# Optimization experiments

Hardware: AMD Instinct MI355X
Metric: run time of the kernel (lower is better)

The kernel has to match this reference:

```python
import jax, jax.numpy as jnp
import numpy as np

T, B, D, FF, Z = 1024, 32, 512, 2048, 64


def _trunc_normal(key, shape, std=0.001):
    return std * jax.random.truncated_normal(key, -2.0, 2.0, shape, dtype=jnp.float32)


def setup_inputs() -> dict:
    key = jax.random.key(0)
    ks = jax.random.split(key, 16)
    inp = {
        "x": jax.random.normal(ks[0], (T, B, D), dtype=jnp.float32),
        "first": jax.random.bernoulli(ks[1], 0.05, (T, B)),  # episode boundaries
        "h0": jax.random.normal(ks[2], (B, D), dtype=jnp.float32),
        "c0": jax.random.normal(ks[3], (B, D), dtype=jnp.float32),
        # pre-LN params
        "ln_g": jnp.ones((D,), jnp.float32),
        "ln_b": jnp.zeros((D,), jnp.float32),
        # LSTM params (PyTorch gate order i,f,g,o)
        "Wih": jax.random.normal(ks[4], (4 * D, D), jnp.float32) / np.sqrt(D),
        "Whh": jax.random.normal(ks[5], (4 * D, D), jnp.float32) / np.sqrt(D),
        "bih": jnp.zeros((4 * D,), jnp.float32),
        "bhh": jnp.zeros((4 * D,), jnp.float32),
        # pointwise FFN: mlp0 = Linear(D,FF)+ReLU, mlp1 = Linear(FF,D)
        "mlp0_w": jax.random.normal(ks[6], (FF, D), jnp.float32) / np.sqrt(D),
        "mlp0_b": jnp.zeros((FF,), jnp.float32),
        "mlp1_w": jax.random.normal(ks[7], (D, FF), jnp.float32) / np.sqrt(FF),
        "mlp1_b": jnp.zeros((D,), jnp.float32),
        # adapter bottleneck (trunc-normal init, std=0.001)
        "aw0": _trunc_normal(ks[8], (Z, D)),
        "ab0": _trunc_normal(ks[9], (Z,)),
        "aw1": _trunc_normal(ks[10], (D, Z)),
        "ab1": _trunc_normal(ks[11], (D,)),
    }
    return inp


def _layernorm(x, g, b, eps=1e-5):
    mu = jnp.mean(x, axis=-1, keepdims=True)
    var = jnp.mean(jnp.square(x - mu), axis=-1, keepdims=True)
    return (x - mu) * jax.lax.rsqrt(var + eps) * g + b


def _lstm_scan(x, first, h0, c0, Wih, Whh, bih, bhh):
    # x: [T,B,D], first: [T,B] bool resets state before the step
    def step(carry, inp):
        h, c = carry
        xt, ft = inp
        keep = jnp.where(ft, 0.0, 1.0)[:, None].astype(h.dtype)
        h = h * keep
        c = c * keep
        gates = xt @ Wih.T + bih + h @ Whh.T + bhh  # [B,4D]
        i, f, g, o = jnp.split(gates, 4, axis=-1)
        c = jax.nn.sigmoid(f) * c + jax.nn.sigmoid(i) * jnp.tanh(g)
        h = jax.nn.sigmoid(o) * jnp.tanh(c)
        return (h, c), h
    (h, c), ys = jax.lax.scan(step, (h0, c0), (x, first))
    return ys, h, c


def reference(x, first, h0, c0, ln_g, ln_b, Wih, Whh, bih, bhh,
              mlp0_w, mlp0_b, mlp1_w, mlp1_b, aw0, ab0, aw1, ab1):
    residual = x
    xn = _layernorm(x, ln_g, ln_b)
    y, h_out, c_out = _lstm_scan(xn, first, h0, c0, Wih, Whh, bih, bhh)
    y = y + residual  # is_residual and 'lstm' in recurrence_type
    residual = y
    # pointwise layer: mlp1(mlp0(y)) with mlp0 = Linear+ReLU
    y = jax.nn.relu(y @ mlp0_w.T + mlp0_b) @ mlp1_w.T + mlp1_b
    # adapter: y + net(y)
    y = y + jax.nn.relu(y @ aw0.T + ab0) @ aw1.T + ab1
    y = y + residual
    return (y, h_out, c_out)
```

## Files before the change

kernel.cpp:

```cpp
#include <hip/hip_runtime.h>

#define T_ 1024
#define B_ 32
#define D_ 512
#define FF_ 2048
#define TB_ 32768
#define TCH_ 256
#define RCH_ 8192

typedef short bf16x8 __attribute__((ext_vector_type(8)));
typedef float f32x4 __attribute__((ext_vector_type(4)));

static __device__ __forceinline__ unsigned int pack2bf(float a, float b){
  union { __bf16 h[2]; unsigned int u; } z;
  z.h[0] = (__bf16)a; z.h[1] = (__bf16)b; return z.u;
}
static __device__ __forceinline__ float bflo(unsigned int u){ return __uint_as_float(u<<16); }
static __device__ __forceinline__ float bfhi(unsigned int u){ return __uint_as_float(u & 0xffff0000u); }
static __device__ __forceinline__ float sigm(float x){ return 1.f/(1.f+__expf(-x)); }
static __device__ __forceinline__ float tanh_(float x){ return 1.f - 2.f/(1.f+__expf(2.f*x)); }

static __device__ __forceinline__ bool firstval(const void* p, int mode, int idx){
  return mode ? (((const int*)p)[idx] != 0) : (((const unsigned char*)p)[idx] != 0);
}

__global__ void detect_first_kernel(const unsigned char* __restrict__ p, unsigned int* __restrict__ mode){
  __shared__ int found;
  if (threadIdx.x == 0) found = 0;
  __syncthreads();
  int f = 0;
  for (int i = threadIdx.x; i < TB_; i += 256) if ((i & 3) != 0 && p[i] != 0) f = 1;
  if (f) atomicAdd(&found, 1);
  __syncthreads();
  if (threadIdx.x == 0) *mode = (found == 0) ? 1u : 0u;
}

__global__ void convert_w_kernel(const float* __restrict__ Wih, const float* __restrict__ Whh,
                                 const float* __restrict__ m0w, const float* __restrict__ m1w,
                                 const float* __restrict__ aw0, const float* __restrict__ aw1,
                                 __bf16* __restrict__ Wihb, __bf16* __restrict__ Whhb,
                                 __bf16* __restrict__ m0b,  __bf16* __restrict__ m1b,
                                 __bf16* __restrict__ awT0, __bf16* __restrict__ awT1){
  int bid = blockIdx.x;
  if (bid < 4096) {
    int ai = bid >> 10;
    size_t off = (size_t)(bid & 1023) * 1024 + threadIdx.x * 4;
    const float* src = (ai==0)?Wih:(ai==1)?Whh:(ai==2)?m0w:m1w;
    __bf16* dst = (ai==0)?Wihb:(ai==1)?Whhb:(ai==2)?m0b:m1b;
    float4 v = *(const float4*)(src + off);
    union { __bf16 h[4]; uint2 u; } z;
    z.h[0]=(__bf16)v.x; z.h[1]=(__bf16)v.y; z.h[2]=(__bf16)v.z; z.h[3]=(__bf16)v.w;
    *(uint2*)(void*)(dst + off) = z.u;
  } else {
    int e = (bid - 4096) * 256 + threadIdx.x;
    if (e < 32768) { int k = e >> 6, j = e & 63;  awT0[e] = (__bf16)aw0[j*512 + k]; }
    else { int e2 = e - 32768; int j = e2 >> 9, d = e2 & 511; awT1[e2] = (__bf16)aw1[d*64 + j]; }
  }
}

__global__ __launch_bounds__(256) void ln_kernel(const float* __restrict__ x,
                                                 const float* __restrict__ g, const float* __restrict__ b,
                                                 __bf16* __restrict__ xn){
  const int w = threadIdx.x >> 6, l = threadIdx.x & 63;
  const int row = blockIdx.x * 4 + w;
  const float* xr = x + (size_t)row * D_;
  const int e0 = l * 4, e1 = 256 + l * 4;
  float4 v0 = *(const float4*)(xr + e0);
  float4 v1 = *(const float4*)(xr + e1);
  float s  = v0.x+v0.y+v0.z+v0.w + v1.x+v1.y+v1.z+v1.w;
  float s2 = v0.x*v0.x+v0.y*v0.y+v0.z*v0.z+v0.w*v0.w + v1.x*v1.x+v1.y*v1.y+v1.z*v1.z+v1.w*v1.w;
  #pragma unroll
  for (int off = 1; off < 64; off <<= 1) { s += __shfl_xor(s, off); s2 += __shfl_xor(s2, off); }
  float mu = s * (1.f/512.f);
  float var = s2 * (1.f/512.f) - mu*mu;
  float rstd = rsqrtf(var + 1e-5f);
  float4 g0 = *(const float4*)(g + e0), g1 = *(const float4*)(g + e1);
  float4 b0 = *(const float4*)(b + e0), b1 = *(const float4*)(b + e1);
  union { __bf16 h[4]; uint2 u; } o0, o1;
  o0.h[0]=(__bf16)((v0.x-mu)*rstd*g0.x+b0.x); o0.h[1]=(__bf16)((v0.y-mu)*rstd*g0.y+b0.y);
  o0.h[2]=(__bf16)((v0.z-mu)*rstd*g0.z+b0.z); o0.h[3]=(__bf16)((v0.w-mu)*rstd*g0.w+b0.w);
  o1.h[0]=(__bf16)((v1.x-mu)*rstd*g1.x+b1.x); o1.h[1]=(__bf16)((v1.y-mu)*rstd*g1.y+b1.y);
  o1.h[2]=(__bf16)((v1.z-mu)*rstd*g1.z+b1.z); o1.h[3]=(__bf16)((v1.w-mu)*rstd*g1.w+b1.w);
  *(uint2*)(void*)(xn + (size_t)row * D_ + e0) = o0.u;
  *(uint2*)(void*)(xn + (size_t)row * D_ + e1) = o1.u;
}

template<int RELU, int BF16OUT, int TWOBIAS>
__global__ __launch_bounds__(256) void gemm_bt(const __bf16* __restrict__ A, const __bf16* __restrict__ W,
                                               const float* __restrict__ bias0, const float* __restrict__ bias1,
                                               float* __restrict__ Cf, __bf16* __restrict__ Cb,
                                               int M, int N, int K){
  __shared__ __bf16 As[128*64];
  __shared__ __bf16 Bs[128*64];
  const int tid = threadIdx.x, w = tid >> 6, l = tid & 63;
  const int bm = blockIdx.x, bn = blockIdx.y;
  const int wm = (w >> 1) * 64, wn = (w & 1) * 64;
  const int nk = K >> 6;

  uint4 ra[4], rb[4];
  #pragma unroll
  for (int i = 0; i < 4; ++i) {
    int s = tid + (i << 8); int row = s >> 3; int ks = s & 7;
    ra[i] = *(const uint4*)(void*)(A + (size_t)(bm*128 + row) * K + ks*8);
    rb[i] = *(const uint4*)(void*)(W + (size_t)(bn*128 + row) * K + ks*8);
  }
  f32x4 acc[4][4];
  #pragma unroll
  for (int mt = 0; mt < 4; ++mt)
    #pragma unroll
    for (int nt = 0; nt < 4; ++nt) acc[mt][nt] = (f32x4){0.f,0.f,0.f,0.f};

  for (int kt = 0; kt < nk; ++kt) {
    __syncthreads();
    #pragma unroll
    for (int i = 0; i < 4; ++i) {
      int s = tid + (i << 8); int row = s >> 3; int ks = s & 7;
      int wi = row * 64 + ((ks * 8) ^ ((row & 7) << 3));
      *(uint4*)(void*)(As + wi) = ra[i];
      *(uint4*)(void*)(Bs + wi) = rb[i];
    }
    __syncthreads();
    if (kt + 1 < nk) {
      #pragma unroll
      for (int i = 0; i < 4; ++i) {
        int s = tid + (i << 8); int row = s >> 3; int ks = s & 7;
        ra[i] = *(const uint4*)(void*)(A + (size_t)(bm*128 + row) * K + (kt+1)*64 + ks*8);
        rb[i] = *(const uint4*)(void*)(W + (size_t)(bn*128 + row) * K + (kt+1)*64 + ks*8);
      }
    }
    #pragma unroll
    for (int kk = 0; kk < 2; ++kk) {
      bf16x8 af[4], bfv[4];
      const int ke = kk * 32 + ((l >> 4) << 3);
      #pragma unroll
      for (int mt = 0; mt < 4; ++mt) {
        int row = wm + mt*16 + (l & 15);
        af[mt] = *(const bf16x8*)(void*)(As + row*64 + (ke ^ ((row & 7) << 3)));
      }
      #pragma unroll
      for (int nt = 0; nt < 4; ++nt) {
        int row = wn + nt*16 + (l & 15);
        bfv[nt] = *(const bf16x8*)(void*)(Bs + row*64 + (ke ^ ((row & 7) << 3)));
      }
      #pragma unroll
      for (int mt = 0; mt < 4; ++mt)
        #pragma unroll
        for (int nt = 0; nt < 4; ++nt)
          acc[mt][nt] = __builtin_amdgcn_mfma_f32_16x16x32_bf16(af[mt], bfv[nt], acc[mt][nt], 0, 0, 0);
    }
  }
  #pragma unroll
  for (int nt = 0; nt < 4; ++nt) {
    int c = bn*128 + wn + nt*16 + (l & 15);
    float bv = bias0[c];
    if (TWOBIAS) bv += bias1[c];
    #pragma unroll
    for (int mt = 0; mt < 4; ++mt) {
      #pragma unroll
      for (int j = 0; j < 4; ++j) {
        int r = bm*128 + wm + mt*16 + ((l >> 4) << 2) + j;
        float v = acc[mt][nt][j] + bv;
        if (RELU) v = fmaxf(v, 0.f);
        if (BF16OUT) Cb[(size_t)r * N + c] = (__bf16)v;
        else         Cf[(size_t)r * N + c] = v;
      }
    }
  }
}

__global__ __launch_bounds__(512) void lstm_scan(
    const __bf16* __restrict__ Whh,
    const __bf16* __restrict__ preC,
    const float*  __restrict__ x,
    const void*   __restrict__ firstp,
    const float*  __restrict__ h0,
    const float*  __restrict__ c0,
    float*        __restrict__ cstate,
    __bf16*       __restrict__ ymidbC,
    unsigned long long* __restrict__ HP,
    const unsigned int* __restrict__ modep,
    float* __restrict__ hout, float* __restrict__ cout,
    int tBase){
  const int s = blockIdx.x, tid = threadIdx.x, w = tid >> 6, l = tid & 63;
  const int d0 = s * 32;
  __shared__ __bf16 Hl[32 * 512];
  __shared__ float  gl[32 * 132];
  const int mode = (int)*modep;

  bf16x8 wf[16];
  {
    int rl = w*16 + (l & 15);
    int gr = (rl >> 5) * 512 + d0 + (rl & 31);
    const __bf16* base = Whh + (size_t)gr * 512 + ((l >> 4) << 3);
    #pragma unroll
    for (int kt = 0; kt < 16; ++kt) wf[kt] = *(const bf16x8*)(void*)(base + kt*32);
  }
  const int b = tid >> 4, dl2 = (tid & 15) * 2;
  const int dg = d0 + dl2;
  const int opid = b * 256 + s * 16 + (tid & 15);

  float cr[2];
  if (tBase == 0) {
    float k0 = firstval(firstp, mode, b) ? 0.f : 1.f;
    float2 c2 = *(const float2*)(c0 + (size_t)b*512 + dg);
    cr[0] = c2.x * k0; cr[1] = c2.y * k0;
    float2 h = *(const float2*)(h0 + (size_t)b*512 + dg);
    unsigned long long pkt = (1ULL << 32) | (unsigned long long)pack2bf(h.x*k0, h.y*k0);
    __hip_atomic_store(HP + opid, pkt, __ATOMIC_RELAXED, __HIP_MEMORY_SCOPE_AGENT);
  } else {
    float2 c2 = *(const float2*)(cstate + (size_t)b*512 + dg);
    cr[0] = c2.x; cr[1] = c2.y;
  }

  for (int tl = 0; tl < TCH_; ++tl) {
    const int t = tBase + tl;
    const int rowg = t * 32 + b, rowl = tl * 32 + b;
    unsigned int pg[4];
    #pragma unroll
    for (int gi = 0; gi < 4; ++gi)
      pg[gi] = *(const unsigned int*)(void*)(preC + (size_t)rowl * 2048 + gi*512 + dg);
    float2 xv = *(const float2*)(x + (size_t)rowg * 512 + dg);
    const bool f_t1 = (t < T_-1) ? firstval(firstp, mode, rowg + 32) : false;

    const unsigned want = (unsigned)(t + 1);
    const unsigned long long* Pb = HP + ((size_t)(t & 1) << 13);
    unsigned long long pk[16];
    #pragma unroll
    for (int j = 0; j < 16; ++j)
      pk[j] = __hip_atomic_load(Pb + tid + (j << 9), __ATOMIC_RELAXED, __HIP_MEMORY_SCOPE_AGENT);
    while (true) {
      unsigned stale = 0;
      #pragma unroll
      for (int j = 0; j < 16; ++j)
        if ((unsigned)(pk[j] >> 32) != want) stale |= (1u << j);
      if (!stale) break;
      __builtin_amdgcn_s_sleep(1);
      #pragma unroll
      for (int j = 0; j < 16; ++j)
        if (stale & (1u << j))
          pk[j] = __hip_atomic_load(Pb + tid + (j << 9), __ATOMIC_RELAXED, __HIP_MEMORY_SCOPE_AGENT);
    }
    #pragma unroll
    for (int j = 0; j < 16; ++j) {
      int pid = tid + (j << 9);
      int pb = pid >> 8, ps = (pid >> 4) & 15, pi = pid & 15;
      int q = ps*32 + pi*2;
      *(unsigned int*)(void*)(Hl + pb*512 + (q ^ ((pb & 7) << 3))) = (unsigned)pk[j];
    }
    __syncthreads();

    f32x4 a0a = (f32x4){0.f,0.f,0.f,0.f}, a0b = (f32x4){0.f,0.f,0.f,0.f};
    f32x4 a1a = (f32x4){0.f,0.f,0.f,0.f}, a1b = (f32x4){0.f,0.f,0.f,0.f};
    #pragma unroll
    for (int kt = 0; kt < 16; kt += 2) {
      int ke0 = kt*32 + ((l >> 4) << 3), ke1 = (kt+1)*32 + ((l >> 4) << 3);
      int r0 = (l & 15), r1 = 16 + (l & 15);
      bf16x8 h00 = *(const bf16x8*)(void*)(Hl + r0*512 + (ke0 ^ ((r0 & 7) << 3)));
      bf16x8 h01 = *(const bf16x8*)(void*)(Hl + r0*512 + (ke1 ^ ((r0 & 7) << 3)));
      bf16x8 h10 = *(const bf16x8*)(void*)(Hl + r1*512 + (ke0 ^ ((r1 & 7) << 3)));
      bf16x8 h11 = *(const bf16x8*)(void*)(Hl + r1*512 + (ke1 ^ ((r1 & 7) << 3)));
      a0a = __builtin_amdgcn_mfma_f32_16x16x32_bf16(h00, wf[kt],   a0a, 0, 0, 0);
      a0b = __builtin_amdgcn_mfma_f32_16x16x32_bf16(h01, wf[kt+1], a0b, 0, 0, 0);
      a1a = __builtin_amdgcn_mfma_f32_16x16x32_bf16(h10, wf[kt],   a1a, 0, 0, 0);
      a1b = __builtin_amdgcn_mfma_f32_16x16x32_bf16(h11, wf[kt+1], a1b, 0, 0, 0);
    }
    f32x4 acc0 = a0a + a0b, acc1 = a1a + a1b;
    {
      int col = w*16 + (l & 15);
      #pragma unroll
      for (int j = 0; j < 4; ++j) {
        gl[(((l >> 4) << 2) + j) * 132 + col]        = acc0[j];
        gl[((16 + ((l >> 4) << 2) + j)) * 132 + col] = acc1[j];
      }
    }
    __syncthreads();

    float2 gv[4];
    #pragma unroll
    for (int gi = 0; gi < 4; ++gi) gv[gi] = *(const float2*)(gl + b*132 + gi*32 + dl2);
    const float keep1 = f_t1 ? 0.f : 1.f;
    float hh[2], cc[2];
    #pragma unroll
    for (int p = 0; p < 2; ++p) {
      float gi_ = (p ? gv[0].y : gv[0].x) + (p ? bfhi(pg[0]) : bflo(pg[0]));
      float gf_ = (p ? gv[1].y : gv[1].x) + (p ? bfhi(pg[1]) : bflo(pg[1]));
      float gg_ = (p ? gv[2].y : gv[2].x) + (p ? bfhi(pg[2]) : bflo(pg[2]));
      float go_ = (p ? gv[3].y : gv[3].x) + (p ? bfhi(pg[3]) : bflo(pg[3]));
      float cn = sigm(gf_) * cr[p] + sigm(gi_) * tanh_(gg_);
      float h  = sigm(go_) * tanh_(cn);
      cc[p] = cn; hh[p] = h;
    }
    cr[0] = cc[0] * keep1; cr[1] = cc[1] * keep1;
    float2 yv = { hh[0] + xv.x, hh[1] + xv.y };
    if (t < T_-1) {
      unsigned long long pkt = (((unsigned long long)(unsigned)(t + 2)) << 32)
                             | (unsigned long long)pack2bf(hh[0]*keep1, hh[1]*keep1);
      __hip_atomic_store(HP + (((size_t)((t+1) & 1)) << 13) + opid, pkt,
                         __ATOMIC_RELAXED, __HIP_MEMORY_SCOPE_AGENT);
      if (tl == TCH_-1) *(float2*)(cstate + (size_t)b*512 + dg) = make_float2(cr[0], cr[1]);
    } else {
      *(float2*)(hout + (size_t)b*512 + dg) = make_float2(hh[0], hh[1]);
      *(float2*)(cout + (size_t)b*512 + dg) = make_float2(cc[0], cc[1]);
    }
    *(unsigned int*)(void*)(ymidbC + (size_t)rowl * 512 + dg) = pack2bf(yv.x, yv.y);
  }
}

__global__ __launch_bounds__(256) void adapter_out_kernel(
    float* __restrict__ y2,
    const __bf16* __restrict__ ymidb,
    const __bf16* __restrict__ awT0,
    const __bf16* __restrict__ awT1,
    const float* __restrict__ ab0, const float* __restrict__ ab1){
  __shared__ float zl[16 * 64];
  const int w = threadIdx.x >> 6, l = threadIdx.x & 63;
  const int r0 = blockIdx.x * 16;
  const float bz = ab0[l];
  #pragma unroll
  for (int rr = 0; rr < 4; ++rr) {
    int rowl = w*4 + rr;
    const float* yr = y2 + (size_t)(r0 + rowl) * 512;
    float acc = bz;
    #pragma unroll 4
    for (int k = 0; k < 512; ++k) acc += yr[k] * (float)awT0[k*64 + l];
    zl[rowl*64 + l] = fmaxf(acc, 0.f);
  }
  __syncthreads();
  #pragma unroll
  for (int rr = 0; rr < 4; ++rr) {
    int rowl = w*4 + rr; int row = r0 + rowl;
    const float* yr = y2  + (size_t)row * 512;
    const __bf16* mr = ymidb + (size_t)row * 512;
    #pragma unroll
    for (int dd = 0; dd < 8; ++dd) {
      int d = dd*64 + l;
      float acc = ab1[d] + yr[d] + (float)mr[d];
      #pragma unroll 4
      for (int j = 0; j < 64; ++j) acc += zl[rowl*64 + j] * (float)awT1[j*512 + d];
      y2[(size_t)row * 512 + d] = acc;
    }
  }
}

extern "C" void kernel_launch(void* const* d_in, const int* in_sizes, int n_in,
                              void* d_out, int out_size, void* d_ws, size_t ws_size,
                              hipStream_t stream){
  (void)in_sizes; (void)n_in; (void)out_size; (void)ws_size;
  const float* x    = (const float*)d_in[0];
  const void*  first=               d_in[1];
  const float* h0   = (const float*)d_in[2];
  const float* c0   = (const float*)d_in[3];
  const float* ln_g = (const float*)d_in[4];
  const float* ln_b = (const float*)d_in[5];
  const float* Wih  = (const float*)d_in[6];
  const float* Whh  = (const float*)d_in[7];
  const float* bih  = (const float*)d_in[8];
  const float* bhh  = (const float*)d_in[9];
  const float* m0w  = (const float*)d_in[10];
  const float* m0b  = (const float*)d_in[11];
  const float* m1w  = (const float*)d_in[12];
  const float* m1b  = (const float*)d_in[13];
  const float* aw0  = (const float*)d_in[14];
  const float* ab0  = (const float*)d_in[15];
  const float* aw1  = (const float*)d_in[16];
  const float* ab1  = (const float*)d_in[17];

  char* ws = (char*)d_ws;
  __bf16* buf0  = (__bf16*)(ws + 0LL);
  __bf16* xnbfC = (__bf16*)(ws + 33554432LL);
  __bf16* ymidbC= (__bf16*)(ws + 41943040LL);
  __bf16* wihb  = (__bf16*)(ws + 50331648LL);
  __bf16* whhb  = (__bf16*)(ws + 52428800LL);
  __bf16* m0bf  = (__bf16*)(ws + 54525952LL);
  __bf16* m1bf  = (__bf16*)(ws + 56623104LL);
  __bf16* awT0  = (__bf16*)(ws + 58720256LL);
  __bf16* awT1  = (__bf16*)(ws + 58785792LL);
  unsigned long long* HP = (unsigned long long*)(ws + 58851328LL);
  float*  cstate= (float*) (ws + 58982400LL);
  unsigned int* mode = (unsigned int*)(ws + 59047936LL);
  __bf16* preC = buf0;
  __bf16* a1C  = buf0;

  float* out  = (float*)d_out;
  float* hout = out + (size_t)TB_ * D_;
  float* cout = hout + B_ * D_;

  hipMemsetAsync(HP, 0, 131072, stream);
  detect_first_kernel<<<1, 256, 0, stream>>>((const unsigned char*)first, mode);
  convert_w_kernel<<<4352, 256, 0, stream>>>(Wih, Whh, m0w, m1w, aw0, aw1,
                                             wihb, whhb, m0bf, m1bf, awT0, awT1);
  for (int c = 0; c < 4; ++c) {
    const size_t ro = (size_t)c * RCH_;
    ln_kernel<<<RCH_/4, 256, 0, stream>>>(x + ro * D_, ln_g, ln_b, xnbfC);
    gemm_bt<0,1,1><<<dim3(RCH_/128, FF_/128), 256, 0, stream>>>(xnbfC, wihb, bih, bhh,
                                                                nullptr, preC, RCH_, 2048, 512);
    lstm_scan<<<16, 512, 0, stream>>>(whhb, preC, x, first, h0, c0, cstate, ymidbC,
                                      HP, mode, hout, cout, c * TCH_);
    gemm_bt<1,1,0><<<dim3(RCH_/128, FF_/128), 256, 0, stream>>>(ymidbC, m0bf, m0b, nullptr,
                                                                nullptr, a1C, RCH_, FF_, 512);
    gemm_bt<0,0,0><<<dim3(RCH_/128, D_/128), 256, 0, stream>>>(a1C, m1bf, m1b, nullptr,
                                                               out + ro * D_, nullptr, RCH_, D_, FF_);
    adapter_out_kernel<<<RCH_/16, 256, 0, stream>>>(out + ro * D_, ymidbC, awT0, awT1, ab0, ab1);
  }
}
```

Baseline: 5.378 ms.

## Overlap LSTM scan with previous chunk FFN and next chunk input GEMM

Fuses the per-chunk pipeline into one persistent-style launch. Blocks 0-15 run the recurrent scan for chunk c, blocks 16-79 run the FFN and adapter for chunk c-1, and blocks 80-143 compute layernorm plus the input projection for chunk c+1, with double-buffered workspace. LayerNorm is folded into the input GEMM's A-tile load, and the FFN panel chains both GEMMs and the adapter per 128-row panel. The aim is to hide the latency-bound scan behind the throughput-bound GEMMs, at the cost of 64-block GEMMs with low parallelism that may compete with the scan blocks, and a workspace-size fallback path.

```diff
diff --git a/kernel.cpp b/kernel.cpp
--- a/kernel.cpp
+++ b/kernel.cpp
@@ -10,6 +10,12 @@
 
 typedef short bf16x8 __attribute__((ext_vector_type(8)));
 typedef float f32x4 __attribute__((ext_vector_type(4)));
+
+union SharedU {
+  struct { __bf16 Hl[32*512]; float gl[32*132]; } s;
+  struct { __bf16 As[128*64]; __bf16 Bs[128*64]; float stat[256]; } g;
+  float zl[128*64];
+};
 
 static __device__ __forceinline__ unsigned int pack2bf(float a, float b){
   union { __bf16 h[2]; unsigned int u; } z;
@@ -58,79 +64,85 @@
   }
 }
 
-__global__ __launch_bounds__(256) void ln_kernel(const float* __restrict__ x,
-                                                 const float* __restrict__ g, const float* __restrict__ b,
-                                                 __bf16* __restrict__ xn){
-  const int w = threadIdx.x >> 6, l = threadIdx.x & 63;
-  const int row = blockIdx.x * 4 + w;
-  const float* xr = x + (size_t)row * D_;
-  const int e0 = l * 4, e1 = 256 + l * 4;
-  float4 v0 = *(const float4*)(xr + e0);
-  float4 v1 = *(const float4*)(xr + e1);
-  float s  = v0.x+v0.y+v0.z+v0.w + v1.x+v1.y+v1.z+v1.w;
-  float s2 = v0.x*v0.x+v0.y*v0.y+v0.z*v0.z+v0.w*v0.w + v1.x*v1.x+v1.y*v1.y+v1.z*v1.z+v1.w*v1.w;
+template<int RELU,int BF16OUT,int TWOBIAS,int AMODE>
+static __device__ void tile_gemm(SharedU& sh,
+    const __bf16* A, const float* Ax, const float* lng, const float* lnb,
+    const __bf16* W, const float* bias0, const float* bias1,
+    float* Cf, __bf16* Cb, int aRow0, int cRow0, int bn, int N, int K){
+  __bf16* As = sh.g.As; __bf16* Bs = sh.g.Bs; const float* stat = sh.g.stat;
+  const int tid = threadIdx.x, w = tid >> 6, l = tid & 63;
+  const int wm = (w >> 2) * 64, wn = (w & 3) * 32;
+  const int nk = K >> 6;
+  uint4 ra[2], rb[2];
+  float4 rx[2][2];
   #pragma unroll
-  for (int off = 1; off < 64; off <<= 1) { s += __shfl_xor(s, off); s2 += __shfl_xor(s2, off); }
-  float mu = s * (1.f/512.f);
-  float var = s2 * (1.f/512.f) - mu*mu;
-  float rstd = rsqrtf(var + 1e-5f);
-  float4 g0 = *(const float4*)(g + e0), g1 = *(const float4*)(g + e1);
-  float4 b0 = *(const float4*)(b + e0), b1 = *(const float4*)(b + e1);
-  union { __bf16 h[4]; uint2 u; } o0, o1;
-  o0.h[0]=(__bf16)((v0.x-mu)*rstd*g0.x+b0.x); o0.h[1]=(__bf16)((v0.y-mu)*rstd*g0.y+b0.y);
-  o0.h[2]=(__bf16)((v0.z-mu)*rstd*g0.z+b0.z); o0.h[3]=(__bf16)((v0.w-mu)*rstd*g0.w+b0.w);
-  o1.h[0]=(__bf16)((v1.x-mu)*rstd*g1.x+b1.x); o1.h[1]=(__bf16)((v1.y-mu)*rstd*g1.y+b1.y);
-  o1.h[2]=(__bf16)((v1.z-mu)*rstd*g1.z+b1.z); o1.h[3]=(__bf16)((v1.w-mu)*rstd*g1.w+b1.w);
-  *(uint2*)(void*)(xn + (size_t)row * D_ + e0) = o0.u;
-  *(uint2*)(void*)(xn + (size_t)row * D_ + e1) = o1.u;
-}
-
-template<int RELU, int BF16OUT, int TWOBIAS>
-__global__ __launch_bounds__(256) void gemm_bt(const __bf16* __restrict__ A, const __bf16* __restrict__ W,
-                                               const float* __restrict__ bias0, const float* __restrict__ bias1,
-                                               float* __restrict__ Cf, __bf16* __restrict__ Cb,
-                                               int M, int N, int K){
-  __shared__ __bf16 As[128*64];
-  __shared__ __bf16 Bs[128*64];
-  const int tid = threadIdx.x, w = tid >> 6, l = tid & 63;
-  const int bm = blockIdx.x, bn = blockIdx.y;
-  const int wm = (w >> 1) * 64, wn = (w & 1) * 64;
-  const int nk = K >> 6;
-
-  uint4 ra[4], rb[4];
-  #pragma unroll
-  for (int i = 0; i < 4; ++i) {
-    int s = tid + (i << 8); int row = s >> 3; int ks = s & 7;
-    ra[i] = *(const uint4*)(void*)(A + (size_t)(bm*128 + row) * K + ks*8);
+  for (int i = 0; i < 2; ++i) {
+    int s = tid + (i << 9); int row = s >> 3; int ks = s & 7;
+    if (AMODE == 2) {
+      const float* px = Ax + (size_t)(aRow0 + row) * 512 + ks*8;
+      rx[i][0] = *(const float4*)px; rx[i][1] = *(const float4*)(px + 4);
+    } else if (AMODE == 1) {
+      const unsigned long long* pa = (const unsigned long long*)(void*)(A + (size_t)(aRow0 + row) * K + ks*8);
+      union { unsigned long long q[2]; uint4 u; } z;
+      z.q[0] = __hip_atomic_load(pa,   __ATOMIC_RELAXED, __HIP_MEMORY_SCOPE_AGENT);
+      z.q[1] = __hip_atomic_load(pa+1, __ATOMIC_RELAXED, __HIP_MEMORY_SCOPE_AGENT);
+      ra[i] = z.u;
+    } else {
+      ra[i] = *(const uint4*)(void*)(A + (size_t)(aRow0 + row) * K + ks*8);
+    }
     rb[i] = *(const uint4*)(void*)(W + (size_t)(bn*128 + row) * K + ks*8);
   }
-  f32x4 acc[4][4];
+  f32x4 acc[4][2];
   #pragma unroll
   for (int mt = 0; mt < 4; ++mt)
     #pragma unroll
-    for (int nt = 0; nt < 4; ++nt) acc[mt][nt] = (f32x4){0.f,0.f,0.f,0.f};
+    for (int nt = 0; nt < 2; ++nt) acc[mt][nt] = (f32x4){0.f,0.f,0.f,0.f};
 
   for (int kt = 0; kt < nk; ++kt) {
     __syncthreads();
     #pragma unroll
-    for (int i = 0; i < 4; ++i) {
-      int s = tid + (i << 8); int row = s >> 3; int ks = s & 7;
+    for (int i = 0; i < 2; ++i) {
+      int s = tid + (i << 9); int row = s >> 3; int ks = s & 7;
       int wi = row * 64 + ((ks * 8) ^ ((row & 7) << 3));
-      *(uint4*)(void*)(As + wi) = ra[i];
+      if (AMODE == 2) {
+        float mu = stat[row], rs = stat[128 + row];
+        int col = kt*64 + ks*8;
+        float4 g0 = *(const float4*)(lng + col), g1 = *(const float4*)(lng + col + 4);
+        float4 b0 = *(const float4*)(lnb + col), b1 = *(const float4*)(lnb + col + 4);
+        union { __bf16 h[8]; uint4 u; } z;
+        z.h[0]=(__bf16)((rx[i][0].x-mu)*rs*g0.x+b0.x); z.h[1]=(__bf16)((rx[i][0].y-mu)*rs*g0.y+b0.y);
+        z.h[2]=(__bf16)((rx[i][0].z-mu)*rs*g0.z+b0.z); z.h[3]=(__bf16)((rx[i][0].w-mu)*rs*g0.w+b0.w);
+        z.h[4]=(__bf16)((rx[i][1].x-mu)*rs*g1.x+b1.x); z.h[5]=(__bf16)((rx[i][1].y-mu)*rs*g1.y+b1.y);
+        z.h[6]=(__bf16)((rx[i][1].z-mu)*rs*g1.z+b1.z); z.h[7]=(__bf16)((rx[i][1].w-mu)*rs*g1.w+b1.w);
+        *(uint4*)(void*)(As + wi) = z.u;
+      } else {
+        *(uint4*)(void*)(As + wi) = ra[i];
+      }
       *(uint4*)(void*)(Bs + wi) = rb[i];
     }
     __syncthreads();
     if (kt + 1 < nk) {
       #pragma unroll
-      for (int i = 0; i < 4; ++i) {
-        int s = tid + (i << 8); int row = s >> 3; int ks = s & 7;
-        ra[i] = *(const uint4*)(void*)(A + (size_t)(bm*128 + row) * K + (kt+1)*64 + ks*8);
+      for (int i = 0; i < 2; ++i) {
+        int s = tid + (i << 9); int row = s >> 3; int ks = s & 7;
+        if (AMODE == 2) {
+          const float* px = Ax + (size_t)(aRow0 + row) * 512 + (kt+1)*64 + ks*8;
+          rx[i][0] = *(const float4*)px; rx[i][1] = *(const float4*)(px + 4);
+        } else if (AMODE == 1) {
+          const unsigned long long* pa = (const unsigned long long*)(void*)(A + (size_t)(aRow0 + row) * K + (kt+1)*64 + ks*8);
+          union { unsigned long long q[2]; uint4 u; } z;
+          z.q[0] = __hip_atomic_load(pa,   __ATOMIC_RELAXED, __HIP_MEMORY_SCOPE_AGENT);
+          z.q[1] = __hip_atomic_load(pa+1, __ATOMIC_RELAXED, __HIP_MEMORY_SCOPE_AGENT);
+          ra[i] = z.u;
+        } else {
+          ra[i] = *(const uint4*)(void*)(A + (size_t)(aRow0 + row) * K + (kt+1)*64 + ks*8);
+        }
         rb[i] = *(const uint4*)(void*)(W + (size_t)(bn*128 + row) * K + (kt+1)*64 + ks*8);
       }
     }
     #pragma unroll
     for (int kk = 0; kk < 2; ++kk) {
-      bf16x8 af[4], bfv[4];
+      bf16x8 af[4], bfv[2];
       const int ke = kk * 32 + ((l >> 4) << 3);
       #pragma unroll
       for (int mt = 0; mt < 4; ++mt) {
@@ -138,19 +150,19 @@
         af[mt] = *(const bf16x8*)(void*)(As + row*64 + (ke ^ ((row & 7) << 3)));
       }
       #pragma unroll
-      for (int nt = 0; nt < 4; ++nt) {
+      for (int nt = 0; nt < 2; ++nt) {
         int row = wn + nt*16 + (l & 15);
         bfv[nt] = *(const bf16x8*)(void*)(Bs + row*64 + (ke ^ ((row & 7) << 3)));
       }
       #pragma unroll
       for (int mt = 0; mt < 4; ++mt)
         #pragma unroll
-        for (int nt = 0; nt < 4; ++nt)
+        for (int nt = 0; nt < 2; ++nt)
           acc[mt][nt] = __builtin_amdgcn_mfma_f32_16x16x32_bf16(af[mt], bfv[nt], acc[mt][nt], 0, 0, 0);
     }
   }
   #pragma unroll
-  for (int nt = 0; nt < 4; ++nt) {
+  for (int nt = 0; nt < 2; ++nt) {
     int c = bn*128 + wn + nt*16 + (l & 15);
     float bv = bias0[c];
     if (TWOBIAS) bv += bias1[c];
@@ -158,7 +170,7 @@
     for (int mt = 0; mt < 4; ++mt) {
       #pragma unroll
       for (int j = 0; j < 4; ++j) {
-        int r = bm*128 + wm + mt*16 + ((l >> 4) << 2) + j;
+        int r = cRow0 + wm + mt*16 + ((l >> 4) << 2) + j;
         float v = acc[mt][nt][j] + bv;
         if (RELU) v = fmaxf(v, 0.f);
         if (BF16OUT) Cb[(size_t)r * N + c] = (__bf16)v;
@@ -168,24 +180,84 @@
   }
 }
 
-__global__ __launch_bounds__(512) void lstm_scan(
-    const __bf16* __restrict__ Whh,
-    const __bf16* __restrict__ preC,
-    const float*  __restrict__ x,
-    const void*   __restrict__ firstp,
-    const float*  __restrict__ h0,
-    const float*  __restrict__ c0,
-    float*        __restrict__ cstate,
-    __bf16*       __restrict__ ymidbC,
-    unsigned long long* __restrict__ HP,
-    const unsigned int* __restrict__ modep,
-    float* __restrict__ hout, float* __restrict__ cout,
-    int tBase){
-  const int s = blockIdx.x, tid = threadIdx.x, w = tid >> 6, l = tid & 63;
+static __device__ void pre_panel(SharedU& sh, int panel, const float* x,
+                                 const float* lng, const float* lnb,
+                                 const __bf16* wihb, const float* bih, const float* bhh,
+                                 __bf16* preOut, int chunkRow0){
+  const int tid = threadIdx.x, w = tid >> 6, l = tid & 63;
+  const int r0 = panel * 128;
+  for (int rr = 0; rr < 16; ++rr) {
+    int rowl = w*16 + rr;
+    const float* xr = x + (size_t)(chunkRow0 + r0 + rowl) * 512 + l*8;
+    float4 v0 = *(const float4*)xr, v1 = *(const float4*)(xr + 4);
+    float s  = v0.x+v0.y+v0.z+v0.w + v1.x+v1.y+v1.z+v1.w;
+    float s2 = v0.x*v0.x+v0.y*v0.y+v0.z*v0.z+v0.w*v0.w + v1.x*v1.x+v1.y*v1.y+v1.z*v1.z+v1.w*v1.w;
+    #pragma unroll
+    for (int off = 1; off < 64; off <<= 1) { s += __shfl_xor(s, off); s2 += __shfl_xor(s2, off); }
+    if (l == 0) {
+      float mu = s * (1.f/512.f);
+      float var = s2 * (1.f/512.f) - mu*mu;
+      sh.g.stat[rowl] = mu; sh.g.stat[128 + rowl] = rsqrtf(var + 1e-5f);
+    }
+  }
+  __syncthreads();
+  for (int bn = 0; bn < 16; ++bn)
+    tile_gemm<0,1,1,2>(sh, nullptr, x, lng, lnb, wihb, bih, bhh,
+                       nullptr, preOut, chunkRow0 + r0, r0, bn, 2048, 512);
+}
+
+static __device__ void ffn_panel(SharedU& sh, int panel, const __bf16* ymidb,
+                                 const __bf16* m0bf, const float* m0b,
+                                 const __bf16* m1bf, const float* m1b,
+                                 __bf16* a1, float* y2,
+                                 const __bf16* awT0, const __bf16* awT1,
+                                 const float* ab0, const float* ab1){
+  const int tid = threadIdx.x, w = tid >> 6, l = tid & 63;
+  const int r0 = panel * 128;
+  for (int bn = 0; bn < 16; ++bn)
+    tile_gemm<1,1,0,0>(sh, ymidb, nullptr, nullptr, nullptr, m0bf, m0b, nullptr,
+                       nullptr, a1, r0, r0, bn, 2048, 512);
+  __syncthreads();
+  for (int bn = 0; bn < 4; ++bn)
+    tile_gemm<0,0,0,1>(sh, a1, nullptr, nullptr, nullptr, m1bf, m1b, nullptr,
+                       y2, nullptr, r0, r0, bn, 512, 2048);
+  __syncthreads();
+  const float bz = ab0[l];
+  for (int rr = 0; rr < 16; ++rr) {
+    int rowl = w*16 + rr; int row = r0 + rowl;
+    const unsigned long long* yp = (const unsigned long long*)(void*)(y2 + (size_t)row * 512);
+    float acc = bz;
+    #pragma unroll 4
+    for (int k2 = 0; k2 < 256; ++k2) {
+      union { unsigned long long q; float f[2]; } z;
+      z.q = __hip_atomic_load(yp + k2, __ATOMIC_RELAXED, __HIP_MEMORY_SCOPE_AGENT);
+      acc += z.f[0]*(float)awT0[(k2*2)*64 + l] + z.f[1]*(float)awT0[(k2*2+1)*64 + l];
+    }
+    sh.zl[rowl*64 + l] = fmaxf(acc, 0.f);
+  }
+  __syncthreads();
+  for (int rr = 0; rr < 16; ++rr) {
+    int rowl = w*16 + rr; int row = r0 + rowl;
+    #pragma unroll
+    for (int dd = 0; dd < 8; ++dd) {
+      int d = dd*64 + l;
+      float yv = __uint_as_float(__hip_atomic_load((const unsigned int*)(void*)(y2 + (size_t)row*512 + d),
+                                                   __ATOMIC_RELAXED, __HIP_MEMORY_SCOPE_AGENT));
+      float acc = ab1[d] + yv + (float)ymidb[(size_t)row*512 + d];
+      #pragma unroll 4
+      for (int j = 0; j < 64; ++j) acc += sh.zl[rowl*64 + j] * (float)awT1[j*512 + d];
+      y2[(size_t)row*512 + d] = acc;
+    }
+  }
+}
+
+static __device__ void scan_core(SharedU& sh, int s,
+    const __bf16* Whh, const __bf16* preC, const float* x, const void* firstp,
+    const float* h0, const float* c0, float* cstate, __bf16* ymidbC,
+    unsigned long long* HP, int mode, float* hout, float* cout, int tBase){
+  const int tid = threadIdx.x, w = tid >> 6, l = tid & 63;
   const int d0 = s * 32;
-  __shared__ __bf16 Hl[32 * 512];
-  __shared__ float  gl[32 * 132];
-  const int mode = (int)*modep;
+  __bf16* Hl = sh.s.Hl; float* gl = sh.s.gl;
 
   bf16x8 wf[16];
   {
@@ -306,46 +378,60 @@
   }
 }
 
-__global__ __launch_bounds__(256) void adapter_out_kernel(
-    float* __restrict__ y2,
+__global__ __launch_bounds__(512) void fused_scan(
+    const __bf16* __restrict__ Whh, const __bf16* __restrict__ preCur,
+    const float* __restrict__ x, const void* __restrict__ firstp,
+    const float* __restrict__ h0, const float* __restrict__ c0,
+    float* __restrict__ cstate, __bf16* __restrict__ ymidbCur,
+    unsigned long long* __restrict__ HP, const unsigned int* __restrict__ modep,
+    float* __restrict__ hout, float* __restrict__ cout, int tBase,
+    int doFfn, const __bf16* __restrict__ ymidbPrev,
+    const __bf16* __restrict__ m0bf, const float* __restrict__ m0b,
+    const __bf16* __restrict__ m1bf, const float* __restrict__ m1b,
+    __bf16* __restrict__ a1, float* __restrict__ outPrev,
+    const __bf16* __restrict__ awT0, const __bf16* __restrict__ awT1,
+    const float* __restrict__ ab0, const float* __restrict__ ab1,
+    int doPre, const float* __restrict__ lng, const float* __restrict__ lnb,
+    const __bf16* __restrict__ wihb, const float* __restrict__ bih, const float* __restrict__ bhh,
+    __bf16* __restrict__ preNext, int nextRow0){
+  __shared__ SharedU sh;
+  const int bid = blockIdx.x;
+  if (bid < 16) {
+    scan_core(sh, bid, Whh, preCur, x, firstp, h0, c0, cstate, ymidbCur,
+              HP, (int)*modep, hout, cout, tBase);
+  } else if (bid < 80) {
+    if (!doFfn) return;
+    ffn_panel(sh, bid - 16, ymidbPrev, m0bf, m0b, m1bf, m1b, a1, outPrev,
+              awT0, awT1, ab0, ab1);
+  } else if (bid < 144) {
+    if (!doPre) return;
+    pre_panel(sh, bid - 80, x, lng, lnb, wihb, bih, bhh, preNext, nextRow0);
+  }
+}
+
+__global__ __launch_bounds__(512) void pre_kernel(
+    const float* __restrict__ x, const float* __restrict__ lng, const float* __restrict__ lnb,
+    const __bf16* __restrict__ wihb, const float* __restrict__ bih, const float* __restrict__ bhh,
+    __bf16* __restrict__ preOut, int chunkRow0){
+  __shared__ SharedU sh;
+  pre_panel(sh, blockIdx.x, x, lng, lnb, wihb, bih, bhh, preOut, chunkRow0);
+}
+
+__global__ __launch_bounds__(512) void ffn_kernel(
     const __bf16* __restrict__ ymidb,
-    const __bf16* __restrict__ awT0,
-    const __bf16* __restrict__ awT1,
+    const __bf16* __restrict__ m0bf, const float* __restrict__ m0b,
+    const __bf16* __restrict__ m1bf, const float* __restrict__ m1b,
+    __bf16* __restrict__ a1, float* __restrict__ y2,
+    const __bf16* __restrict__ awT0, const __bf16* __restrict__ awT1,
     const float* __restrict__ ab0, const float* __restrict__ ab1){
-  __shared__ float zl[16 * 64];
-  const int w = threadIdx.x >> 6, l = threadIdx.x & 63;
-  const int r0 = blockIdx.x * 16;
-  const float bz = ab0[l];
-  #pragma unroll
-  for (int rr = 0; rr < 4; ++rr) {
-    int rowl = w*4 + rr;
-    const float* yr = y2 + (size_t)(r0 + rowl) * 512;
-    float acc = bz;
-    #pragma unroll 4
-    for (int k = 0; k < 512; ++k) acc += yr[k] * (float)awT0[k*64 + l];
-    zl[rowl*64 + l] = fmaxf(acc, 0.f);
-  }
-  __syncthreads();
-  #pragma unroll
-  for (int rr = 0; rr < 4; ++rr) {
-    int rowl = w*4 + rr; int row = r0 + rowl;
-    const float* yr = y2  + (size_t)row * 512;
-    const __bf16* mr = ymidb + (size_t)row * 512;
-    #pragma unroll
-    for (int dd = 0; dd < 8; ++dd) {
-      int d = dd*64 + l;
-      float acc = ab1[d] + yr[d] + (float)mr[d];
-      #pragma unroll 4
-      for (int j = 0; j < 64; ++j) acc += zl[rowl*64 + j] * (float)awT1[j*512 + d];
-      y2[(size_t)row * 512 + d] = acc;
-    }
-  }
+  __shared__ SharedU sh;
+  ffn_panel(sh, blockIdx.x, ymidb, m0bf, m0b, m1bf, m1b, a1, y2, awT0, awT1, ab0, ab1);
 }
 
 extern "C" void kernel_launch(void* const* d_in, const int* in_sizes, int n_in,
                               void* d_out, int out_size, void* d_ws, size_t ws_size,
                               hipStream_t stream){
-  (void)in_sizes; (void)n_in; (void)out_size; (void)ws_size;
+  (void)in_sizes; (void)n_in; (void)out_size;
   const float* x    = (const float*)d_in[0];
   const void*  first=               d_in[1];
   const float* h0   = (const float*)d_in[2];
@@ -365,41 +451,75 @@
   const float* aw1  = (const float*)d_in[16];
   const float* ab1  = (const float*)d_in[17];
 
-  char* ws = (char*)d_ws;
-  __bf16* buf0  = (__bf16*)(ws + 0LL);
-  __bf16* xnbfC = (__bf16*)(ws + 33554432LL);
-  __bf16* ymidbC= (__bf16*)(ws + 41943040LL);
-  __bf16* wihb  = (__bf16*)(ws + 50331648LL);
-  __bf16* whhb  = (__bf16*)(ws + 52428800LL);
-  __bf16* m0bf  = (__bf16*)(ws + 54525952LL);
-  __bf16* m1bf  = (__bf16*)(ws + 56623104LL);
-  __bf16* awT0  = (__bf16*)(ws + 58720256LL);
-  __bf16* awT1  = (__bf16*)(ws + 58785792LL);
-  unsigned long long* HP = (unsigned long long*)(ws + 58851328LL);
-  float*  cstate= (float*) (ws + 58982400LL);
-  unsigned int* mode = (unsigned int*)(ws + 59047936LL);
-  __bf16* preC = buf0;
-  __bf16* a1C  = buf0;
-
   float* out  = (float*)d_out;
   float* hout = out + (size_t)TB_ * D_;
   float* cout = hout + B_ * D_;
-
-  hipMemsetAsync(HP, 0, 131072, stream);
-  detect_first_kernel<<<1, 256, 0, stream>>>((const unsigned char*)first, mode);
-  convert_w_kernel<<<4352, 256, 0, stream>>>(Wih, Whh, m0w, m1w, aw0, aw1,
-                                             wihb, whhb, m0bf, m1bf, awT0, awT1);
-  for (int c = 0; c < 4; ++c) {
-    const size_t ro = (size_t)c * RCH_;
-    ln_kernel<<<RCH_/4, 256, 0, stream>>>(x + ro * D_, ln_g, ln_b, xnbfC);
-    gemm_bt<0,1,1><<<dim3(RCH_/128, FF_/128), 256, 0, stream>>>(xnbfC, wihb, bih, bhh,
-                                                                nullptr, preC, RCH_, 2048, 512);
-    lstm_scan<<<16, 512, 0, stream>>>(whhb, preC, x, first, h0, c0, cstate, ymidbC,
-                                      HP, mode, hout, cout, c * TCH_);
-    gemm_bt<1,1,0><<<dim3(RCH_/128, FF_/128), 256, 0, stream>>>(ymidbC, m0bf, m0b, nullptr,
-                                                                nullptr, a1C, RCH_, FF_, 512);
-    gemm_bt<0,0,0><<<dim3(RCH_/128, D_/128), 256, 0, stream>>>(a1C, m1bf, m1b, nullptr,
-                                                               out + ro * D_, nullptr, RCH_, D_, FF_);
-    adapter_out_kernel<<<RCH_/16, 256, 0, stream>>>(out + ro * D_, ymidbC, awT0, awT1, ab0, ab1);
-  }
-}
+  char* ws = (char*)d_ws;
+
+  const bool planA = (ws_size >= (size_t)126160000ULL);
+
+  if (planA) {
+    __bf16* preA  = (__bf16*)(ws + 0LL);
+    __bf16* preB  = (__bf16*)(ws + 33554432LL);
+    __bf16* a1b   = (__bf16*)(ws + 67108864LL);
+    __bf16* ymA   = (__bf16*)(ws + 100663296LL);
+    __bf16* ymB   = (__bf16*)(ws + 109051904LL);
+    __bf16* wihb  = (__bf16*)(ws + 117440512LL);
+    __bf16* whhb  = (__bf16*)(ws + 119537664LL);
+    __bf16* m0bf  = (__bf16*)(ws + 121634816LL);
+    __bf16* m1bf  = (__bf16*)(ws + 123731968LL);
+    __bf16* awT0  = (__bf16*)(ws + 125829120LL);
+    __bf16* awT1  = (__bf16*)(ws + 125894656LL);
+    unsigned long long* HP = (unsigned long long*)(ws + 125960192LL);
+    float*  cstate= (float*) (ws + 126091264LL);
+    unsigned int* mode = (unsigned int*)(ws + 126156800LL);
+
+    hipMemsetAsync(HP, 0, 131072, stream);
+    detect_first_kernel<<<1, 256, 0, stream>>>((const unsigned char*)first, mode);
+    convert_w_kernel<<<4352, 256, 0, stream>>>(Wih, Whh, m0w, m1w, aw0, aw1,
+                                               wihb, whhb, m0bf, m1bf, awT0, awT1);
+    pre_kernel<<<64, 512, 0, stream>>>(x, ln_g, ln_b, wihb, bih, bhh, preA, 0);
+    for (int c = 0; c < 4; ++c) {
+      __bf16* preCur  = (c & 1) ? preB : preA;
+      __bf16* preNext = (c & 1) ? preA : preB;
+      __bf16* ymCur   = (c & 1) ? ymB : ymA;
+      __bf16* ymPrev  = (c & 1) ? ymA : ymB;
+      int doFfn = (c > 0), doPre = (c < 3);
+      fused_scan<<<144, 512, 0, stream>>>(
+          whhb, preCur, x, first, h0, c0, cstate, ymCur, HP, mode, hout, cout, c * TCH_,
+          doFfn, ymPrev, m0bf, m0b, m1bf, m1b, a1b, out + (size_t)(c-1) * RCH_ * D_,
+          awT0, awT1, ab0, ab1,
+          doPre, ln_g, ln_b, wihb, bih, bhh, preNext, (c+1) * RCH_);
+    }
+    ffn_kernel<<<64, 512, 0, stream>>>(ymB, m0bf, m0b, m1bf, m1b, a1b,
+                                       out + (size_t)3 * RCH_ * D_, awT0, awT1, ab0, ab1);
+  } else {
+    __bf16* preS  = (__bf16*)(ws + 0LL);
+    __bf16* a1b   = preS;
+    __bf16* ymC   = (__bf16*)(ws + 33554432LL);
+    __bf16* wihb  = (__bf16*)(ws + 41943040LL);
+    __bf16* whhb  = (__bf16*)(ws + 44040192LL);
+    __bf16* m0bf  = (__bf16*)(ws + 46137344LL);
+    __bf16* m1bf  = (__bf16*)(ws + 48234496LL);
+    __bf16* awT0  = (__bf16*)(ws + 50331648LL);
+    __bf16* awT1  = (__bf16*)(ws + 50397184LL);
+    unsigned long long* HP = (unsigned long long*)(ws + 50462720LL);
+    float*  cstate= (float*) (ws + 50593792LL);
+    unsigned int* mode = (unsigned int*)(ws + 50659328LL);
+
+    hipMemsetAsync(HP, 0, 131072, stream);
+    detect_first_kernel<<<1, 256, 0, stream>>>((const unsigned char*)first, mode);
+    convert_w_kernel<<<4352, 256, 0, stream>>>(Wih, Whh, m0w, m1w, aw0, aw1,
+                                               wihb, whhb, m0bf, m1bf, awT0, awT1);
+    for (int c = 0; c < 4; ++c) {
+      pre_kernel<<<64, 512, 0, stream>>>(x, ln_g, ln_b, wihb, bih, bhh, preS, c * RCH_);
+      fused_scan<<<16, 512, 0, stream>>>(
+          whhb, preS, x, first, h0, c0, cstate, ymC, HP, mode, hout, cout, c * TCH_,
+          0, nullptr, nullptr, nullptr, nullptr, nullptr, nullptr, nullptr,
+          nullptr, nullptr, nullptr, nullptr,
+          0, nullptr, nullptr, nullptr, nullptr, nullptr, nullptr, 0);
+      ffn_kernel<<<64, 512, 0, stream>>>(ymC, m0bf, m0b, m1bf, m1b, a1b,
+                                         out + (size_t)c * RCH_ * D_, awT0, awT1, ab0, ab1);
+    }
+  }
+}
```

After: 6.894 ms. 28.2% more time.

## Fuse input projection into LSTM scan and run scan over full sequence

Applied to the files above, without the earlier changes.

Removes the separate input-projection GEMM and the precomputed gate buffer. Each scan step now computes the x·Wih contribution with MFMA inside the recurrent kernel before it waits on the hidden-state exchange, so that work can overlap the spin wait. The four-chunk pipeline is replaced by one full-length scan followed by two larger MLP GEMM passes and a single adapter launch. The trade-off is that the Wih fragments and normalized inputs are reloaded from global or cache on every step of the serial scan, which may lengthen the critical path. Removing the chunks also loses any overlap between chunks and needs a larger workspace.

```diff
diff --git a/kernel.cpp b/kernel.cpp
--- a/kernel.cpp
+++ b/kernel.cpp
@@ -5,8 +5,6 @@
 #define D_ 512
 #define FF_ 2048
 #define TB_ 32768
-#define TCH_ 256
-#define RCH_ 8192
 
 typedef short bf16x8 __attribute__((ext_vector_type(8)));
 typedef float f32x4 __attribute__((ext_vector_type(4)));
@@ -15,8 +13,6 @@
   union { __bf16 h[2]; unsigned int u; } z;
   z.h[0] = (__bf16)a; z.h[1] = (__bf16)b; return z.u;
 }
-static __device__ __forceinline__ float bflo(unsigned int u){ return __uint_as_float(u<<16); }
-static __device__ __forceinline__ float bfhi(unsigned int u){ return __uint_as_float(u & 0xffff0000u); }
 static __device__ __forceinline__ float sigm(float x){ return 1.f/(1.f+__expf(-x)); }
 static __device__ __forceinline__ float tanh_(float x){ return 1.f - 2.f/(1.f+__expf(2.f*x)); }
 
@@ -85,9 +81,9 @@
   *(uint2*)(void*)(xn + (size_t)row * D_ + e1) = o1.u;
 }
 
-template<int RELU, int BF16OUT, int TWOBIAS>
+template<int RELU, int BF16OUT>
 __global__ __launch_bounds__(256) void gemm_bt(const __bf16* __restrict__ A, const __bf16* __restrict__ W,
-                                               const float* __restrict__ bias0, const float* __restrict__ bias1,
+                                               const float* __restrict__ bias0,
                                                float* __restrict__ Cf, __bf16* __restrict__ Cb,
                                                int M, int N, int K){
   __shared__ __bf16 As[128*64];
@@ -153,7 +149,6 @@
   for (int nt = 0; nt < 4; ++nt) {
     int c = bn*128 + wn + nt*16 + (l & 15);
     float bv = bias0[c];
-    if (TWOBIAS) bv += bias1[c];
     #pragma unroll
     for (int mt = 0; mt < 4; ++mt) {
       #pragma unroll
@@ -170,55 +165,56 @@
 
 __global__ __launch_bounds__(512) void lstm_scan(
     const __bf16* __restrict__ Whh,
-    const __bf16* __restrict__ preC,
+    const __bf16* __restrict__ Wih,
+    const __bf16* __restrict__ xnb,
     const float*  __restrict__ x,
     const void*   __restrict__ firstp,
     const float*  __restrict__ h0,
     const float*  __restrict__ c0,
-    float*        __restrict__ cstate,
-    __bf16*       __restrict__ ymidbC,
+    const float*  __restrict__ bih,
+    const float*  __restrict__ bhh,
+    __bf16*       __restrict__ ymidb,
     unsigned long long* __restrict__ HP,
     const unsigned int* __restrict__ modep,
-    float* __restrict__ hout, float* __restrict__ cout,
-    int tBase){
+    float* __restrict__ hout, float* __restrict__ cout){
   const int s = blockIdx.x, tid = threadIdx.x, w = tid >> 6, l = tid & 63;
   const int d0 = s * 32;
   __shared__ __bf16 Hl[32 * 512];
   __shared__ float  gl[32 * 132];
   const int mode = (int)*modep;
 
+  const int rl = w*16 + (l & 15);
+  const int gr = (rl >> 5) * 512 + d0 + (rl & 31);
   bf16x8 wf[16];
   {
-    int rl = w*16 + (l & 15);
-    int gr = (rl >> 5) * 512 + d0 + (rl & 31);
     const __bf16* base = Whh + (size_t)gr * 512 + ((l >> 4) << 3);
     #pragma unroll
     for (int kt = 0; kt < 16; ++kt) wf[kt] = *(const bf16x8*)(void*)(base + kt*32);
   }
+  const __bf16* wib = Wih + (size_t)gr * 512 + ((l >> 4) << 3);
   const int b = tid >> 4, dl2 = (tid & 15) * 2;
   const int dg = d0 + dl2;
   const int opid = b * 256 + s * 16 + (tid & 15);
 
+  float2 bsum[4];
+  #pragma unroll
+  for (int gi = 0; gi < 4; ++gi) {
+    int idx = gi*512 + dg;
+    bsum[gi] = make_float2(bih[idx] + bhh[idx], bih[idx+1] + bhh[idx+1]);
+  }
+
   float cr[2];
-  if (tBase == 0) {
+  {
     float k0 = firstval(firstp, mode, b) ? 0.f : 1.f;
     float2 c2 = *(const float2*)(c0 + (size_t)b*512 + dg);
     cr[0] = c2.x * k0; cr[1] = c2.y * k0;
     float2 h = *(const float2*)(h0 + (size_t)b*512 + dg);
     unsigned long long pkt = (1ULL << 32) | (unsigned long long)pack2bf(h.x*k0, h.y*k0);
     __hip_atomic_store(HP + opid, pkt, __ATOMIC_RELAXED, __HIP_MEMORY_SCOPE_AGENT);
-  } else {
-    float2 c2 = *(const float2*)(cstate + (size_t)b*512 + dg);
-    cr[0] = c2.x; cr[1] = c2.y;
-  }
-
-  for (int tl = 0; tl < TCH_; ++tl) {
-    const int t = tBase + tl;
-    const int rowg = t * 32 + b, rowl = tl * 32 + b;
-    unsigned int pg[4];
-    #pragma unroll
-    for (int gi = 0; gi < 4; ++gi)
-      pg[gi] = *(const unsigned int*)(void*)(preC + (size_t)rowl * 2048 + gi*512 + dg);
+  }
+
+  for (int t = 0; t < T_; ++t) {
+    const int rowg = t * 32 + b;
     float2 xv = *(const float2*)(x + (size_t)rowg * 512 + dg);
     const bool f_t1 = (t < T_-1) ? firstval(firstp, mode, rowg + 32) : false;
 
@@ -228,6 +224,27 @@
     #pragma unroll
     for (int j = 0; j < 16; ++j)
       pk[j] = __hip_atomic_load(Pb + tid + (j << 9), __ATOMIC_RELAXED, __HIP_MEMORY_SCOPE_AGENT);
+
+    f32x4 a0a = (f32x4){0.f,0.f,0.f,0.f}, a0b = (f32x4){0.f,0.f,0.f,0.f};
+    f32x4 a1a = (f32x4){0.f,0.f,0.f,0.f}, a1b = (f32x4){0.f,0.f,0.f,0.f};
+    {
+      const __bf16* xr0 = xnb + (size_t)(t*32 + (l & 15)) * 512 + ((l >> 4) << 3);
+      const __bf16* xr1 = xr0 + 16*512;
+      #pragma unroll
+      for (int kt = 0; kt < 16; kt += 2) {
+        bf16x8 wi0 = *(const bf16x8*)(void*)(wib + kt*32);
+        bf16x8 wi1 = *(const bf16x8*)(void*)(wib + (kt+1)*32);
+        bf16x8 x00 = *(const bf16x8*)(void*)(xr0 + kt*32);
+        bf16x8 x01 = *(const bf16x8*)(void*)(xr0 + (kt+1)*32);
+        bf16x8 x10 = *(const bf16x8*)(void*)(xr1 + kt*32);
+        bf16x8 x11 = *(const bf16x8*)(void*)(xr1 + (kt+1)*32);
+        a0a = __builtin_amdgcn_mfma_f32_16x16x32_bf16(x00, wi0, a0a, 0, 0, 0);
+        a0b = __builtin_amdgcn_mfma_f32_16x16x32_bf16(x01, wi1, a0b, 0, 0, 0);
+        a1a = __builtin_amdgcn_mfma_f32_16x16x32_bf16(x10, wi0, a1a, 0, 0, 0);
+        a1b = __builtin_amdgcn_mfma_f32_16x16x32_bf16(x11, wi1, a1b, 0, 0, 0);
+      }
+    }
+
     while (true) {
       unsigned stale = 0;
       #pragma unroll
@@ -249,8 +266,6 @@
     }
     __syncthreads();
 
-    f32x4 a0a = (f32x4){0.f,0.f,0.f,0.f}, a0b = (f32x4){0.f,0.f,0.f,0.f};
-    f32x4 a1a = (f32x4){0.f,0.f,0.f,0.f}, a1b = (f32x4){0.f,0.f,0.f,0.f};
     #pragma unroll
     for (int kt = 0; kt < 16; kt += 2) {
       int ke0 = kt*32 + ((l >> 4) << 3), ke1 = (kt+1)*32 + ((l >> 4) << 3);
@@ -282,10 +297,10 @@
     float hh[2], cc[2];
     #pragma unroll
     for (int p = 0; p < 2; ++p) {
-      float gi_ = (p ? gv[0].y : gv[0].x) + (p ? bfhi(pg[0]) : bflo(pg[0]));
-      float gf_ = (p ? gv[1].y : gv[1].x) + (p ? bfhi(pg[1]) : bflo(pg[1]));
-      float gg_ = (p ? gv[2].y : gv[2].x) + (p ? bfhi(pg[2]) : bflo(pg[2]));
-      float go_ = (p ? gv[3].y : gv[3].x) + (p ? bfhi(pg[3]) : bflo(pg[3]));
+      float gi_ = (p ? gv[0].y : gv[0].x) + (p ? bsum[0].y : bsum[0].x);
+      float gf_ = (p ? gv[1].y : gv[1].x) + (p ? bsum[1].y : bsum[1].x);
+      float gg_ = (p ? gv[2].y : gv[2].x) + (p ? bsum[2].y : bsum[2].x);
+      float go_ = (p ? gv[3].y : gv[3].x) + (p ? bsum[3].y : bsum[3].x);
       float cn = sigm(gf_) * cr[p] + sigm(gi_) * tanh_(gg_);
       float h  = sigm(go_) * tanh_(cn);
       cc[p] = cn; hh[p] = h;
@@ -297,12 +312,11 @@
                              | (unsigned long long)pack2bf(hh[0]*keep1, hh[1]*keep1);
       __hip_atomic_store(HP + (((size_t)((t+1) & 1)) << 13) + opid, pkt,
                          __ATOMIC_RELAXED, __HIP_MEMORY_SCOPE_AGENT);
-      if (tl == TCH_-1) *(float2*)(cstate + (size_t)b*512 + dg) = make_float2(cr[0], cr[1]);
     } else {
       *(float2*)(hout + (size_t)b*512 + dg) = make_float2(hh[0], hh[1]);
       *(float2*)(cout + (size_t)b*512 + dg) = make_float2(cc[0], cc[1]);
     }
-    *(unsigned int*)(void*)(ymidbC + (size_t)rowl * 512 + dg) = pack2bf(yv.x, yv.y);
+    *(unsigned int*)(void*)(ymidb + (size_t)rowg * 512 + dg) = pack2bf(yv.x, yv.y);
   }
 }
 
@@ -366,20 +380,17 @@
   const float* ab1  = (const float*)d_in[17];
 
   char* ws = (char*)d_ws;
-  __bf16* buf0  = (__bf16*)(ws + 0LL);
-  __bf16* xnbfC = (__bf16*)(ws + 33554432LL);
-  __bf16* ymidbC= (__bf16*)(ws + 41943040LL);
-  __bf16* wihb  = (__bf16*)(ws + 50331648LL);
-  __bf16* whhb  = (__bf16*)(ws + 52428800LL);
-  __bf16* m0bf  = (__bf16*)(ws + 54525952LL);
-  __bf16* m1bf  = (__bf16*)(ws + 56623104LL);
-  __bf16* awT0  = (__bf16*)(ws + 58720256LL);
-  __bf16* awT1  = (__bf16*)(ws + 58785792LL);
-  unsigned long long* HP = (unsigned long long*)(ws + 58851328LL);
-  float*  cstate= (float*) (ws + 58982400LL);
-  unsigned int* mode = (unsigned int*)(ws + 59047936LL);
-  __bf16* preC = buf0;
-  __bf16* a1C  = buf0;
+  __bf16* xnbf  = (__bf16*)(ws + 0LL);
+  __bf16* a1    = (__bf16*)(ws + 0LL);
+  __bf16* ymidb = (__bf16*)(ws + 67108864LL);
+  __bf16* wihb  = (__bf16*)(ws + 100663296LL);
+  __bf16* whhb  = (__bf16*)(ws + 102760448LL);
+  __bf16* m0bf  = (__bf16*)(ws + 104857600LL);
+  __bf16* m1bf  = (__bf16*)(ws + 106954752LL);
+  __bf16* awT0  = (__bf16*)(ws + 109051904LL);
+  __bf16* awT1  = (__bf16*)(ws + 109117440LL);
+  unsigned long long* HP = (unsigned long long*)(ws + 109182976LL);
+  unsigned int* mode = (unsigned int*)(ws + 109314048LL);
 
   float* out  = (float*)d_out;
   float* hout = out + (size_t)TB_ * D_;
@@ -389,17 +400,15 @@
   detect_first_kernel<<<1, 256, 0, stream>>>((const unsigned char*)first, mode);
   convert_w_kernel<<<4352, 256, 0, stream>>>(Wih, Whh, m0w, m1w, aw0, aw1,
                                              wihb, whhb, m0bf, m1bf, awT0, awT1);
-  for (int c = 0; c < 4; ++c) {
-    const size_t ro = (size_t)c * RCH_;
-    ln_kernel<<<RCH_/4, 256, 0, stream>>>(x + ro * D_, ln_g, ln_b, xnbfC);
-    gemm_bt<0,1,1><<<dim3(RCH_/128, FF_/128), 256, 0, stream>>>(xnbfC, wihb, bih, bhh,
-                                                                nullptr, preC, RCH_, 2048, 512);
-    lstm_scan<<<16, 512, 0, stream>>>(whhb, preC, x, first, h0, c0, cstate, ymidbC,
-                                      HP, mode, hout, cout, c * TCH_);
-    gemm_bt<1,1,0><<<dim3(RCH_/128, FF_/128), 256, 0, stream>>>(ymidbC, m0bf, m0b, nullptr,
-                                                                nullptr, a1C, RCH_, FF_, 512);
-    gemm_bt<0,0,0><<<dim3(RCH_/128, D_/128), 256, 0, stream>>>(a1C, m1bf, m1b, nullptr,
-                                                               out + ro * D_, nullptr, RCH_, D_, FF_);
-    adapter_out_kernel<<<RCH_/16, 256, 0, stream>>>(out + ro * D_, ymidbC, awT0, awT1, ab0, ab1);
-  }
-}
+  ln_kernel<<<TB_/4, 256, 0, stream>>>(x, ln_g, ln_b, xnbf);
+  lstm_scan<<<16, 512, 0, stream>>>(whhb, wihb, xnbf, x, first, h0, c0, bih, bhh,
+                                    ymidb, HP, mode, hout, cout);
+  for (int p = 0; p < 2; ++p) {
+    const size_t ro = (size_t)p * 16384;
+    gemm_bt<1,1><<<dim3(128, FF_/128), 256, 0, stream>>>(ymidb + ro * D_, m0bf, m0b,
+                                                         nullptr, a1, 16384, FF_, D_);
+    gemm_bt<0,0><<<dim3(128, D_/128), 256, 0, stream>>>(a1, m1bf, m1b,
+                                                        out + ro * D_, nullptr, 16384, D_, FF_);
+  }
+  adapter_out_kernel<<<TB_/16, 256, 0, stream>>>(out, ymidb, awT0, awT1, ab0, ab1);
+}
```

Result: slower. 16.43 ms (+205.6%).
